# Optimization experiments

Hardware: AMD Instinct MI355X
Metric: run time of the kernel (lower is better)

The kernel has to match this reference:

```python
import jax, jax.numpy as jnp
import numpy as np

N_NODES = 102400   # 256 graphs x 400 nodes
N_EDGES = 1638400  # avg degree 16
C_IN = 128
C_OUT = 128
N_SAGE = 3         # gnn_num
G = 256            # num graphs
M = 400            # nodes per graph (equal-sized -> to_dense_batch is a reshape)


def setup_inputs() -> dict:
    key = jax.random.key(0)
    ks = jax.random.split(key, 6)
    x = jax.random.normal(ks[0], (N_NODES, C_IN), dtype=jnp.float32)
    edge_index = jax.random.randint(ks[1], (2, N_EDGES), 0, N_NODES, dtype=jnp.int32)
    # nodes sorted by graph id, equal graph sizes (matches to_dense_batch assumptions)
    batch = (jnp.arange(N_NODES, dtype=jnp.int32) // M)
    s_in = 1.0 / np.sqrt(C_IN)
    s_out = 1.0 / np.sqrt(C_OUT)
    W_g = jax.random.normal(ks[2], (C_IN, C_OUT), dtype=jnp.float32) * s_in
    b_g = jnp.zeros((C_OUT,), dtype=jnp.float32)
    W_l = jax.random.normal(ks[3], (N_SAGE, C_OUT, C_OUT), dtype=jnp.float32) * s_out  # neighbor lin
    b_l = jnp.zeros((N_SAGE, C_OUT), dtype=jnp.float32)
    W_r = jax.random.normal(ks[4], (N_SAGE, C_OUT, C_OUT), dtype=jnp.float32) * s_out  # root lin (no bias in PyG)
    return {"x": x, "W_g": W_g, "b_g": b_g, "W_l": W_l, "b_l": b_l,
            "W_r": W_r, "edge_index": edge_index, "batch": batch}


def _gcn_conv(x, W, b, src, dst):
    # PyG GCNConv: h = x W; add self loops; norm = d^{-1/2}_src * d^{-1/2}_dst,
    # deg = in-degree at dst counting the self loop; aggregate at dst; add bias.
    h = x @ W                                                     # [N, C_out]
    ones = jnp.ones((N_EDGES,), dtype=h.dtype)
    deg = jax.ops.segment_sum(ones, dst, num_segments=N_NODES) + 1.0
    dinv = jax.lax.rsqrt(deg)                                     # [N]
    norm = dinv[src] * dinv[dst]                                  # [E]
    agg = jax.ops.segment_sum(h[src] * norm[:, None], dst, num_segments=N_NODES)
    agg = agg + h * (dinv * dinv)[:, None]                        # self-loop term
    return agg + b


def _sage_conv(x, W_l, b_l, W_r, src, dst):
    # PyG SAGEConv (mean aggr): out = mean_{j in N(i)} x_j @ W_l + b_l + x @ W_r
    ones = jnp.ones((N_EDGES,), dtype=x.dtype)
    cnt = jax.ops.segment_sum(ones, dst, num_segments=N_NODES)
    s = jax.ops.segment_sum(x[src], dst, num_segments=N_NODES)
    mean = s / jnp.maximum(cnt, 1.0)[:, None]
    return mean @ W_l + b_l + x @ W_r


def _to_dense(x):
    # equal-sized graphs with nodes sorted by batch -> to_dense_batch == reshape
    return x.reshape(G, M, C_OUT)


def reference(x, W_g, b_g, W_l, b_l, W_r, edge_index, batch):
    src, dst = edge_index[0], edge_index[1]
    x = jax.nn.relu(_gcn_conv(x, W_g, b_g, src, dst))
    outs = [_to_dense(x)]
    for i in range(N_SAGE):
        x = jax.nn.relu(_sage_conv(x, W_l[i], b_l[i], W_r[i], src, dst))
        outs.append(_to_dense(x))
    return jnp.stack(outs)  # [N_SAGE+1, G, M, C_OUT]
```

## Files before the change

kernel.cpp:

```cpp
#include <hip/hip_runtime.h>

#define C 128
#define SLOT 64
typedef __attribute__((ext_vector_type(8))) short bf16x8;
typedef __attribute__((ext_vector_type(4))) float f32x4;

__device__ __forceinline__ unsigned short f2bf_rtn(float f) {
    unsigned u = __float_as_uint(f);
    return (unsigned short)((u + 0x7fff + ((u >> 16) & 1)) >> 16);
}
__device__ __forceinline__ float bflo(unsigned u) { return __uint_as_float(u << 16); }
__device__ __forceinline__ float bfhi(unsigned u) { return __uint_as_float(u & 0xffff0000u); }

__device__ __forceinline__ void gload_lds16(const unsigned short* g, unsigned short* l) {
    __builtin_amdgcn_global_load_lds(
        (const __attribute__((address_space(1))) void*)g,
        (__attribute__((address_space(3))) void*)l, 16, 0, 0);
}

__device__ __forceinline__ void split_bf16(float w, unsigned short& hb, unsigned short& lb) {
    unsigned u = __float_as_uint(w);
    hb = (unsigned short)(u >> 16);
    float hf = __uint_as_float(u & 0xffff0000u);
    lb = (unsigned short)(__float_as_uint(w - hf) >> 16);
}

__global__ __launch_bounds__(256) void wprep_all(const float* __restrict__ Wg,
        const float* __restrict__ Wl, const float* __restrict__ Wr,
        unsigned short* __restrict__ dstG, unsigned short* __restrict__ dstF,
        int* __restrict__ deg, int n) {
    int idx = blockIdx.x * 256 + threadIdx.x;
    if (idx < n) deg[idx] = 0;
    if (idx < 16384) {
        int k64 = idx & 63, ch = (idx >> 6) & 127, chunk = idx >> 13;
        int k = chunk * 64 + k64;
        unsigned short hb, lb;
        split_bf16(Wg[(size_t)k * 128 + ch], hb, lb);
        int pos = (((k64 >> 3) ^ (ch & 7)) << 3) | (k64 & 7);
        size_t base = ((size_t)chunk * 2) * 8192 + ch * 64 + pos;
        dstG[base] = hb;
        dstG[base + 8192] = lb;
    }
    int fidx = idx - 16384;
    if (fidx >= 0 && fidx < 3 * 4 * 128 * 64) {
        int k64 = fidx & 63, ch = (fidx >> 6) & 127, chunk = (fidx >> 13) & 3,
            layer = fidx >> 15;
        int k = chunk * 64 + k64;
        float w = (k < 128) ? Wl[((size_t)layer * 128 + k) * 128 + ch]
                            : Wr[((size_t)layer * 128 + (k - 128)) * 128 + ch];
        int pos = (((k64 >> 3) ^ (ch & 7)) << 3) | (k64 & 7);
        dstF[(((size_t)layer * 4 + chunk)) * 8192 + ch * 64 + pos] = f2bf_rtn(w);
    }
}

__global__ __launch_bounds__(256) void build_gemm_kernel(
        const int* __restrict__ ei, int* __restrict__ deg, int* __restrict__ rank, int E,
        const float* __restrict__ x, const unsigned short* __restrict__ Wp,
        unsigned short* __restrict__ outbf) {
    __shared__ unsigned short Bs[2][128][64];
    const int b2 = blockIdx.x >> 1;
    const int t = threadIdx.x;

    if (!(blockIdx.x & 1)) {
        const int base = b2 * 1024 + t * 4;
        int4 d4 = *(const int4*)(ei + E + base);
        int4 r;
        r.x = atomicAdd(&deg[d4.x], 1);
        r.y = atomicAdd(&deg[d4.y], 1);
        r.z = atomicAdd(&deg[d4.z], 1);
        r.w = atomicAdd(&deg[d4.w], 1);
        *(int4*)(rank + base) = r;
        return;
    }

    unsigned short* BsFlat = &Bs[0][0][0];
    const int lane = t & 63;
    const int wv = t >> 6;
    const int rowbase = b2 * 64 + wv * 16;
    const int arow = rowbase + (lane & 15);
    const int kq = lane >> 4;

    f32x4 acc[8];
#pragma unroll
    for (int f = 0; f < 8; f++) acc[f] = (f32x4){0.f, 0.f, 0.f, 0.f};

#pragma unroll
    for (int c = 0; c < 2; c++) {
        __syncthreads();
        {
            const unsigned short* srcW = Wp + (size_t)c * 16384;
#pragma unroll
            for (int i = 0; i < 8; i++)
                gload_lds16(srcW + (wv * 8 + i) * 512 + lane * 8,
                            BsFlat + (wv * 8 + i) * 512);
        }
        bf16x8 Ah[2], Al[2];
#pragma unroll
        for (int j = 0; j < 2; j++) {
            const float* base = x + (size_t)arow * C + c * 64 + j * 32;
            float4 x0 = ((const float4*)base)[kq * 2];
            float4 x1 = ((const float4*)base)[kq * 2 + 1];
            float xv[8] = {x0.x, x0.y, x0.z, x0.w, x1.x, x1.y, x1.z, x1.w};
#pragma unroll
            for (int q = 0; q < 8; q++) {
                unsigned u = __float_as_uint(xv[q]);
                Ah[j][q] = (short)(u >> 16);
                float hf = __uint_as_float(u & 0xffff0000u);
                Al[j][q] = (short)(__float_as_uint(xv[q] - hf) >> 16);
            }
        }
        __syncthreads();
#pragma unroll
        for (int j = 0; j < 2; j++) {
#pragma unroll
            for (int f = 0; f < 8; f++) {
                const int chh = f * 16 + (lane & 15);
                const int uu = (j * 4 + kq) ^ (lane & 7);
                bf16x8 bh = *(const bf16x8*)&Bs[0][chh][uu * 8];
                bf16x8 bl = *(const bf16x8*)&Bs[1][chh][uu * 8];
                acc[f] = __builtin_amdgcn_mfma_f32_16x16x32_bf16(Ah[j], bh, acc[f], 0, 0, 0);
                acc[f] = __builtin_amdgcn_mfma_f32_16x16x32_bf16(Al[j], bh, acc[f], 0, 0, 0);
                acc[f] = __builtin_amdgcn_mfma_f32_16x16x32_bf16(Ah[j], bl, acc[f], 0, 0, 0);
            }
        }
    }
    const int col = lane & 15;
    const int rq = lane >> 4;
#pragma unroll
    for (int f = 0; f < 8; f++)
#pragma unroll
        for (int j = 0; j < 4; j++) {
            const size_t o = (size_t)(rowbase + rq * 4 + j) * C + f * 16 + col;
            outbf[o] = f2bf_rtn(acc[f][j]);
        }
}

__global__ __launch_bounds__(256) void scatter_scale_kernel(
        const int* __restrict__ ei, const int* __restrict__ rank,
        int* __restrict__ csr, int E, const int* __restrict__ deg,
        unsigned short* __restrict__ tbl, float* __restrict__ dinv,
        float* __restrict__ cinv, int n) {
    const int SB = E >> 10;
    const int t = threadIdx.x;
    if (blockIdx.x < SB) {
        const int base = blockIdx.x * 1024 + t * 4;
        int4 s4 = *(const int4*)(ei + base);
        int4 d4 = *(const int4*)(ei + E + base);
        int4 r4 = *(const int4*)(rank + base);
        if (r4.x < SLOT) csr[(d4.x << 6) + r4.x] = s4.x;
        if (r4.y < SLOT) csr[(d4.y << 6) + r4.y] = s4.y;
        if (r4.z < SLOT) csr[(d4.z << 6) + r4.z] = s4.z;
        if (r4.w < SLOT) csr[(d4.w << 6) + r4.w] = s4.w;
        return;
    }
    const int rb = (blockIdx.x - SB) * 16 + (t >> 4);
    if (rb >= n) return;
    const int ch = (t & 15) * 8;
    const int d = deg[rb];
    const float di = rsqrtf((float)(d + 1));
    if ((t & 15) == 0) {
        dinv[rb] = di;
        cinv[rb] = 1.0f / (float)max(d, 1);
    }
    unsigned short* row = tbl + (size_t)rb * C + ch;
    uint4 v = *(const uint4*)row;
    uint4 w;
    w.x = (unsigned)f2bf_rtn(bflo(v.x) * di) | ((unsigned)f2bf_rtn(bfhi(v.x) * di) << 16);
    w.y = (unsigned)f2bf_rtn(bflo(v.y) * di) | ((unsigned)f2bf_rtn(bfhi(v.y) * di) << 16);
    w.z = (unsigned)f2bf_rtn(bflo(v.z) * di) | ((unsigned)f2bf_rtn(bfhi(v.z) * di) << 16);
    w.w = (unsigned)f2bf_rtn(bflo(v.w) * di) | ((unsigned)f2bf_rtn(bfhi(v.w) * di) << 16);
    *(uint4*)row = w;
}

template<int WBF>
__global__ __launch_bounds__(256) void gemm_sage(
        const unsigned short* __restrict__ Xbf, const unsigned short* __restrict__ Mbf,
        const unsigned short* __restrict__ Wp, const float* __restrict__ bias,
        float* __restrict__ outf, unsigned short* __restrict__ outbf) {
    __shared__ unsigned short Bs[128][64];
    unsigned short* BsFlat = &Bs[0][0];
    const int t = threadIdx.x;
    const int lane = t & 63;
    const int wv = t >> 6;
    const int rowbase = blockIdx.x * 64 + wv * 16;
    const int arow = rowbase + (lane & 15);
    const int kq = lane >> 4;

    f32x4 acc[8];
#pragma unroll
    for (int f = 0; f < 8; f++) acc[f] = (f32x4){0.f, 0.f, 0.f, 0.f};

#pragma unroll
    for (int c = 0; c < 4; c++) {
        __syncthreads();
        {
            const unsigned short* srcW = Wp + (size_t)c * 8192;
#pragma unroll
            for (int i = 0; i < 4; i++)
                gload_lds16(srcW + (wv * 4 + i) * 512 + lane * 8,
                            BsFlat + (wv * 4 + i) * 512);
        }
        const unsigned short* tab = (c < 2) ? Mbf : Xbf;
        bf16x8 Ah[2];
#pragma unroll
        for (int j = 0; j < 2; j++)
            Ah[j] = *(const bf16x8*)(tab + (size_t)arow * C + (c & 1) * 64 + j * 32 + kq * 8);
        __syncthreads();
#pragma unroll
        for (int j = 0; j < 2; j++) {
#pragma unroll
            for (int f = 0; f < 8; f++) {
                const int chh = f * 16 + (lane & 15);
                const int uu = (j * 4 + kq) ^ (lane & 7);
                bf16x8 bh = *(const bf16x8*)&Bs[chh][uu * 8];
                acc[f] = __builtin_amdgcn_mfma_f32_16x16x32_bf16(Ah[j], bh, acc[f], 0, 0, 0);
            }
        }
    }
    const int col = lane & 15;
    const int rq = lane >> 4;
#pragma unroll
    for (int f = 0; f < 8; f++) {
        const float b = bias[f * 16 + col];
#pragma unroll
        for (int j = 0; j < 4; j++) {
            const size_t o = (size_t)(rowbase + rq * 4 + j) * C + f * 16 + col;
            float v = fmaxf(acc[f][j] + b, 0.f);
            outf[o] = v;
            if (WBF) outbf[o] = f2bf_rtn(v);
        }
    }
}

template<int SELF, int BIASRELU, int WF, int WBF>
__global__ __launch_bounds__(256) void agg_kernel(
        const unsigned short* __restrict__ tbl, const int* __restrict__ csr,
        const int* __restrict__ deg, const float* __restrict__ scale,
        const float* __restrict__ bias, float* __restrict__ outf,
        unsigned short* __restrict__ outbf, int n) {
    const int lane = threadIdx.x & 63;
    const int qi = lane & 15;
    const int i = blockIdx.x * 16 + (threadIdx.x >> 6) * 4 + (lane >> 4);
    if (i >= n) return;
    const int dcount = min(deg[i], SLOT);
    const int b = i << 6;
    const int c8 = qi * 8;
    float a0 = 0.f, a1 = 0.f, a2 = 0.f, a3 = 0.f;
    float a4 = 0.f, a5 = 0.f, a6 = 0.f, a7 = 0.f;
#define ACC8(v) do { \
        a0 += bflo(v.x); a1 += bfhi(v.x); a2 += bflo(v.y); a3 += bfhi(v.y); \
        a4 += bflo(v.z); a5 += bfhi(v.z); a6 += bflo(v.w); a7 += bfhi(v.w); } while (0)
    for (int base = 0; base < dcount; base += 16) {
        const int cnt = min(16, dcount - base);
        int idx = (base + qi < dcount) ? csr[b + base + qi] : 0;
        int p = 0;
        for (; p + 8 <= cnt; p += 8) {
            int s0 = __shfl(idx, (lane & 48) + p);
            int s1 = __shfl(idx, (lane & 48) + p + 1);
            int s2 = __shfl(idx, (lane & 48) + p + 2);
            int s3 = __shfl(idx, (lane & 48) + p + 3);
            int s4 = __shfl(idx, (lane & 48) + p + 4);
            int s5 = __shfl(idx, (lane & 48) + p + 5);
            int s6 = __shfl(idx, (lane & 48) + p + 6);
            int s7 = __shfl(idx, (lane & 48) + p + 7);
            uint4 v0 = *(const uint4*)(tbl + (size_t)s0 * C + c8);
            uint4 v1 = *(const uint4*)(tbl + (size_t)s1 * C + c8);
            uint4 v2 = *(const uint4*)(tbl + (size_t)s2 * C + c8);
            uint4 v3 = *(const uint4*)(tbl + (size_t)s3 * C + c8);
            uint4 v4 = *(const uint4*)(tbl + (size_t)s4 * C + c8);
            uint4 v5 = *(const uint4*)(tbl + (size_t)s5 * C + c8);
            uint4 v6 = *(const uint4*)(tbl + (size_t)s6 * C + c8);
            uint4 v7 = *(const uint4*)(tbl + (size_t)s7 * C + c8);
            ACC8(v0); ACC8(v1); ACC8(v2); ACC8(v3);
            ACC8(v4); ACC8(v5); ACC8(v6); ACC8(v7);
        }
        for (; p + 4 <= cnt; p += 4) {
            int s0 = __shfl(idx, (lane & 48) + p);
            int s1 = __shfl(idx, (lane & 48) + p + 1);
            int s2 = __shfl(idx, (lane & 48) + p + 2);
            int s3 = __shfl(idx, (lane & 48) + p + 3);
            uint4 v0 = *(const uint4*)(tbl + (size_t)s0 * C + c8);
            uint4 v1 = *(const uint4*)(tbl + (size_t)s1 * C + c8);
            uint4 v2 = *(const uint4*)(tbl + (size_t)s2 * C + c8);
            uint4 v3 = *(const uint4*)(tbl + (size_t)s3 * C + c8);
            ACC8(v0); ACC8(v1); ACC8(v2); ACC8(v3);
        }
        for (; p < cnt; p++) {
            int s = __shfl(idx, (lane & 48) + p);
            uint4 v = *(const uint4*)(tbl + (size_t)s * C + c8);
            ACC8(v);
        }
    }
#undef ACC8
    if (SELF) {
        uint4 h = *(const uint4*)(tbl + (size_t)i * C + c8);
        a0 += bflo(h.x); a1 += bfhi(h.x); a2 += bflo(h.y); a3 += bfhi(h.y);
        a4 += bflo(h.z); a5 += bfhi(h.z); a6 += bflo(h.w); a7 += bfhi(h.w);
    }
    const float sc = scale[i];
    a0 *= sc; a1 *= sc; a2 *= sc; a3 *= sc;
    a4 *= sc; a5 *= sc; a6 *= sc; a7 *= sc;
    if (BIASRELU) {
        float4 b0 = *(const float4*)(bias + c8);
        float4 b1 = *(const float4*)(bias + c8 + 4);
        a0 = fmaxf(a0 + b0.x, 0.f); a1 = fmaxf(a1 + b0.y, 0.f);
        a2 = fmaxf(a2 + b0.z, 0.f); a3 = fmaxf(a3 + b0.w, 0.f);
        a4 = fmaxf(a4 + b1.x, 0.f); a5 = fmaxf(a5 + b1.y, 0.f);
        a6 = fmaxf(a6 + b1.z, 0.f); a7 = fmaxf(a7 + b1.w, 0.f);
    }
    if (WF) {
        float4 r0; r0.x = a0; r0.y = a1; r0.z = a2; r0.w = a3;
        float4 r1; r1.x = a4; r1.y = a5; r1.z = a6; r1.w = a7;
        *(float4*)(outf + (size_t)i * C + c8) = r0;
        *(float4*)(outf + (size_t)i * C + c8 + 4) = r1;
    }
    if (WBF) {
        uint4 pk;
        pk.x = (unsigned)f2bf_rtn(a0) | ((unsigned)f2bf_rtn(a1) << 16);
        pk.y = (unsigned)f2bf_rtn(a2) | ((unsigned)f2bf_rtn(a3) << 16);
        pk.z = (unsigned)f2bf_rtn(a4) | ((unsigned)f2bf_rtn(a5) << 16);
        pk.w = (unsigned)f2bf_rtn(a6) | ((unsigned)f2bf_rtn(a7) << 16);
        *(uint4*)(outbf + (size_t)i * C + c8) = pk;
    }
}


extern "C" void kernel_launch(void* const* d_in, const int* in_sizes, int n_in,
                              void* d_out, int out_size, void* d_ws, size_t ws_size,
                              hipStream_t stream) {
    const float* x   = (const float*)d_in[0];
    const float* W_g = (const float*)d_in[1];
    const float* b_g = (const float*)d_in[2];
    const float* W_l = (const float*)d_in[3];
    const float* b_l = (const float*)d_in[4];
    const float* W_r = (const float*)d_in[5];
    const int*   ei  = (const int*)d_in[6];

    const int N = in_sizes[0] / C;
    const int E = in_sizes[6] / 2;
    const size_t NC = (size_t)N * C;

    char* ws = (char*)d_ws;
    unsigned short* meanbf = (unsigned short*)ws;
    int* rank = (int*)meanbf;
    unsigned short* tblA   = meanbf + NC;
    unsigned short* tblB   = tblA + NC;
    int* deg  = (int*)(tblB + NC);
    float* dinv = (float*)(deg + N);
    float* cinv = dinv + N;
    unsigned short* wsWg = (unsigned short*)(cinv + N);
    unsigned short* wsWf = wsWg + 32768;

    float* out0 = (float*)d_out;
    int* csr = (int*)(out0 + 3 * NC);

    wprep_all<<<448, 256, 0, stream>>>(W_g, W_l, W_r, wsWg, wsWf, deg, N);

    build_gemm_kernel<<<2 * (N / 64), 256, 0, stream>>>(ei, deg, rank, E,
                                                        x, wsWg, tblA);
    scatter_scale_kernel<<<(E >> 10) + N / 16, 256, 0, stream>>>(
        ei, rank, csr, E, deg, tblA, dinv, cinv, N);

    agg_kernel<1, 1, 1, 1><<<(N + 15) / 16, 256, 0, stream>>>(tblA, csr, deg, dinv,
                                                              b_g, out0, tblB, N);

    const unsigned short* tin[3] = {tblB, tblA, tblB};
    unsigned short* tout[3] = {tblA, tblB, nullptr};
    for (int l = 0; l < 3; l++) {
        float* yout = out0 + (size_t)(l + 1) * NC;
        agg_kernel<0, 0, 0, 1><<<(N + 15) / 16, 256, 0, stream>>>(
            tin[l], csr, deg, cinv, nullptr, nullptr, meanbf, N);
        if (l < 2)
            gemm_sage<1><<<N / 64, 256, 0, stream>>>(tin[l], meanbf,
                wsWf + (size_t)l * 32768, b_l + (size_t)l * C, yout, tout[l]);
        else
            gemm_sage<0><<<N / 64, 256, 0, stream>>>(tin[l], meanbf,
                wsWf + (size_t)l * 32768, b_l + (size_t)l * C, yout, nullptr);
    }
}
```

Baseline: 421.6 us.

## Fuse SAGE mean aggregation into the GEMM kernel via LDS staging

Each SAGE layer now runs a single fused kernel. It gathers neighbor rows for 64 nodes, writes the bf16 mean into a swizzled LDS tile, and feeds that tile straight into the MFMA GEMM. This removes the separate aggregation launch and the global round-trip of the mean buffer. The CSR moves from the output buffer into the workspace, and the GCN aggregation kernel is specialized, dropping its 4-wide remainder loop. In exchange the fused kernel uses more LDS, and the gather and GEMM phases no longer overlap across kernels, which may lower occupancy.

```diff
diff --git a/kernel.cpp b/kernel.cpp
--- a/kernel.cpp
+++ b/kernel.cpp
@@ -172,68 +172,7 @@
     *(uint4*)row = w;
 }
 
-template<int WBF>
-__global__ __launch_bounds__(256) void gemm_sage(
-        const unsigned short* __restrict__ Xbf, const unsigned short* __restrict__ Mbf,
-        const unsigned short* __restrict__ Wp, const float* __restrict__ bias,
-        float* __restrict__ outf, unsigned short* __restrict__ outbf) {
-    __shared__ unsigned short Bs[128][64];
-    unsigned short* BsFlat = &Bs[0][0];
-    const int t = threadIdx.x;
-    const int lane = t & 63;
-    const int wv = t >> 6;
-    const int rowbase = blockIdx.x * 64 + wv * 16;
-    const int arow = rowbase + (lane & 15);
-    const int kq = lane >> 4;
-
-    f32x4 acc[8];
-#pragma unroll
-    for (int f = 0; f < 8; f++) acc[f] = (f32x4){0.f, 0.f, 0.f, 0.f};
-
-#pragma unroll
-    for (int c = 0; c < 4; c++) {
-        __syncthreads();
-        {
-            const unsigned short* srcW = Wp + (size_t)c * 8192;
-#pragma unroll
-            for (int i = 0; i < 4; i++)
-                gload_lds16(srcW + (wv * 4 + i) * 512 + lane * 8,
-                            BsFlat + (wv * 4 + i) * 512);
-        }
-        const unsigned short* tab = (c < 2) ? Mbf : Xbf;
-        bf16x8 Ah[2];
-#pragma unroll
-        for (int j = 0; j < 2; j++)
-            Ah[j] = *(const bf16x8*)(tab + (size_t)arow * C + (c & 1) * 64 + j * 32 + kq * 8);
-        __syncthreads();
-#pragma unroll
-        for (int j = 0; j < 2; j++) {
-#pragma unroll
-            for (int f = 0; f < 8; f++) {
-                const int chh = f * 16 + (lane & 15);
-                const int uu = (j * 4 + kq) ^ (lane & 7);
-                bf16x8 bh = *(const bf16x8*)&Bs[chh][uu * 8];
-                acc[f] = __builtin_amdgcn_mfma_f32_16x16x32_bf16(Ah[j], bh, acc[f], 0, 0, 0);
-            }
-        }
-    }
-    const int col = lane & 15;
-    const int rq = lane >> 4;
-#pragma unroll
-    for (int f = 0; f < 8; f++) {
-        const float b = bias[f * 16 + col];
-#pragma unroll
-        for (int j = 0; j < 4; j++) {
-            const size_t o = (size_t)(rowbase + rq * 4 + j) * C + f * 16 + col;
-            float v = fmaxf(acc[f][j] + b, 0.f);
-            outf[o] = v;
-            if (WBF) outbf[o] = f2bf_rtn(v);
-        }
-    }
-}
-
-template<int SELF, int BIASRELU, int WF, int WBF>
-__global__ __launch_bounds__(256) void agg_kernel(
+__global__ __launch_bounds__(256) void agg_gcn(
         const unsigned short* __restrict__ tbl, const int* __restrict__ csr,
         const int* __restrict__ deg, const float* __restrict__ scale,
         const float* __restrict__ bias, float* __restrict__ outf,
@@ -274,17 +213,6 @@
             ACC8(v0); ACC8(v1); ACC8(v2); ACC8(v3);
             ACC8(v4); ACC8(v5); ACC8(v6); ACC8(v7);
         }
-        for (; p + 4 <= cnt; p += 4) {
-            int s0 = __shfl(idx, (lane & 48) + p);
-            int s1 = __shfl(idx, (lane & 48) + p + 1);
-            int s2 = __shfl(idx, (lane & 48) + p + 2);
-            int s3 = __shfl(idx, (lane & 48) + p + 3);
-            uint4 v0 = *(const uint4*)(tbl + (size_t)s0 * C + c8);
-            uint4 v1 = *(const uint4*)(tbl + (size_t)s1 * C + c8);
-            uint4 v2 = *(const uint4*)(tbl + (size_t)s2 * C + c8);
-            uint4 v3 = *(const uint4*)(tbl + (size_t)s3 * C + c8);
-            ACC8(v0); ACC8(v1); ACC8(v2); ACC8(v3);
-        }
         for (; p < cnt; p++) {
             int s = __shfl(idx, (lane & 48) + p);
             uint4 v = *(const uint4*)(tbl + (size_t)s * C + c8);
@@ -292,35 +220,151 @@
         }
     }
 #undef ACC8
-    if (SELF) {
+    {
         uint4 h = *(const uint4*)(tbl + (size_t)i * C + c8);
         a0 += bflo(h.x); a1 += bfhi(h.x); a2 += bflo(h.y); a3 += bfhi(h.y);
         a4 += bflo(h.z); a5 += bfhi(h.z); a6 += bflo(h.w); a7 += bfhi(h.w);
     }
     const float sc = scale[i];
-    a0 *= sc; a1 *= sc; a2 *= sc; a3 *= sc;
-    a4 *= sc; a5 *= sc; a6 *= sc; a7 *= sc;
-    if (BIASRELU) {
-        float4 b0 = *(const float4*)(bias + c8);
-        float4 b1 = *(const float4*)(bias + c8 + 4);
-        a0 = fmaxf(a0 + b0.x, 0.f); a1 = fmaxf(a1 + b0.y, 0.f);
-        a2 = fmaxf(a2 + b0.z, 0.f); a3 = fmaxf(a3 + b0.w, 0.f);
-        a4 = fmaxf(a4 + b1.x, 0.f); a5 = fmaxf(a5 + b1.y, 0.f);
-        a6 = fmaxf(a6 + b1.z, 0.f); a7 = fmaxf(a7 + b1.w, 0.f);
-    }
-    if (WF) {
-        float4 r0; r0.x = a0; r0.y = a1; r0.z = a2; r0.w = a3;
-        float4 r1; r1.x = a4; r1.y = a5; r1.z = a6; r1.w = a7;
-        *(float4*)(outf + (size_t)i * C + c8) = r0;
-        *(float4*)(outf + (size_t)i * C + c8 + 4) = r1;
-    }
-    if (WBF) {
+    float4 b0 = *(const float4*)(bias + c8);
+    float4 b1 = *(const float4*)(bias + c8 + 4);
+    a0 = fmaxf(a0 * sc + b0.x, 0.f); a1 = fmaxf(a1 * sc + b0.y, 0.f);
+    a2 = fmaxf(a2 * sc + b0.z, 0.f); a3 = fmaxf(a3 * sc + b0.w, 0.f);
+    a4 = fmaxf(a4 * sc + b1.x, 0.f); a5 = fmaxf(a5 * sc + b1.y, 0.f);
+    a6 = fmaxf(a6 * sc + b1.z, 0.f); a7 = fmaxf(a7 * sc + b1.w, 0.f);
+    float4 r0; r0.x = a0; r0.y = a1; r0.z = a2; r0.w = a3;
+    float4 r1; r1.x = a4; r1.y = a5; r1.z = a6; r1.w = a7;
+    *(float4*)(outf + (size_t)i * C + c8) = r0;
+    *(float4*)(outf + (size_t)i * C + c8 + 4) = r1;
+    uint4 pk;
+    pk.x = (unsigned)f2bf_rtn(a0) | ((unsigned)f2bf_rtn(a1) << 16);
+    pk.y = (unsigned)f2bf_rtn(a2) | ((unsigned)f2bf_rtn(a3) << 16);
+    pk.z = (unsigned)f2bf_rtn(a4) | ((unsigned)f2bf_rtn(a5) << 16);
+    pk.w = (unsigned)f2bf_rtn(a6) | ((unsigned)f2bf_rtn(a7) << 16);
+    *(uint4*)(outbf + (size_t)i * C + c8) = pk;
+}
+
+template<int WBF>
+__global__ __launch_bounds__(256, 5) void fused_sage(
+        const unsigned short* __restrict__ tbl, const int* __restrict__ csr,
+        const int* __restrict__ deg, const float* __restrict__ cinv,
+        const unsigned short* __restrict__ Wp, const float* __restrict__ bias,
+        float* __restrict__ outf, unsigned short* __restrict__ outbf) {
+    __shared__ unsigned short Bs[128][64];
+    __shared__ unsigned short meanL[64][128];
+    unsigned short* BsFlat = &Bs[0][0];
+    const int t = threadIdx.x;
+    const int lane = t & 63;
+    const int wv = t >> 6;
+    const int qi = lane & 15;
+    const int qrow = lane >> 4;
+
+    for (int rr = 0; rr < 4; rr++) {
+        const int rloc = wv * 16 + rr * 4 + qrow;
+        const int gi = blockIdx.x * 64 + rloc;
+        const int dcount = min(deg[gi], SLOT);
+        const int b = gi << 6;
+        const int c8 = qi * 8;
+        float a0 = 0.f, a1 = 0.f, a2 = 0.f, a3 = 0.f;
+        float a4 = 0.f, a5 = 0.f, a6 = 0.f, a7 = 0.f;
+#define ACC8(v) do { \
+        a0 += bflo(v.x); a1 += bfhi(v.x); a2 += bflo(v.y); a3 += bfhi(v.y); \
+        a4 += bflo(v.z); a5 += bfhi(v.z); a6 += bflo(v.w); a7 += bfhi(v.w); } while (0)
+        for (int base = 0; base < dcount; base += 16) {
+            const int cnt = min(16, dcount - base);
+            int idx = (base + qi < dcount) ? csr[b + base + qi] : 0;
+            int p = 0;
+            for (; p + 8 <= cnt; p += 8) {
+                int s0 = __shfl(idx, (lane & 48) + p);
+                int s1 = __shfl(idx, (lane & 48) + p + 1);
+                int s2 = __shfl(idx, (lane & 48) + p + 2);
+                int s3 = __shfl(idx, (lane & 48) + p + 3);
+                int s4 = __shfl(idx, (lane & 48) + p + 4);
+                int s5 = __shfl(idx, (lane & 48) + p + 5);
+                int s6 = __shfl(idx, (lane & 48) + p + 6);
+                int s7 = __shfl(idx, (lane & 48) + p + 7);
+                uint4 v0 = *(const uint4*)(tbl + (size_t)s0 * C + c8);
+                uint4 v1 = *(const uint4*)(tbl + (size_t)s1 * C + c8);
+                uint4 v2 = *(const uint4*)(tbl + (size_t)s2 * C + c8);
+                uint4 v3 = *(const uint4*)(tbl + (size_t)s3 * C + c8);
+                uint4 v4 = *(const uint4*)(tbl + (size_t)s4 * C + c8);
+                uint4 v5 = *(const uint4*)(tbl + (size_t)s5 * C + c8);
+                uint4 v6 = *(const uint4*)(tbl + (size_t)s6 * C + c8);
+                uint4 v7 = *(const uint4*)(tbl + (size_t)s7 * C + c8);
+                ACC8(v0); ACC8(v1); ACC8(v2); ACC8(v3);
+                ACC8(v4); ACC8(v5); ACC8(v6); ACC8(v7);
+            }
+            for (; p < cnt; p++) {
+                int s = __shfl(idx, (lane & 48) + p);
+                uint4 v = *(const uint4*)(tbl + (size_t)s * C + c8);
+                ACC8(v);
+            }
+        }
+#undef ACC8
+        const float sc = cinv[gi];
+        a0 *= sc; a1 *= sc; a2 *= sc; a3 *= sc;
+        a4 *= sc; a5 *= sc; a6 *= sc; a7 *= sc;
         uint4 pk;
         pk.x = (unsigned)f2bf_rtn(a0) | ((unsigned)f2bf_rtn(a1) << 16);
         pk.y = (unsigned)f2bf_rtn(a2) | ((unsigned)f2bf_rtn(a3) << 16);
         pk.z = (unsigned)f2bf_rtn(a4) | ((unsigned)f2bf_rtn(a5) << 16);
         pk.w = (unsigned)f2bf_rtn(a6) | ((unsigned)f2bf_rtn(a7) << 16);
-        *(uint4*)(outbf + (size_t)i * C + c8) = pk;
+        *(uint4*)((char*)&meanL[rloc][0] + ((qi ^ (rloc & 7)) << 4)) = pk;
+    }
+
+    const int arow_loc = wv * 16 + (lane & 15);
+    const int arow = blockIdx.x * 64 + arow_loc;
+    const int kq = lane >> 4;
+    const int rowbase = blockIdx.x * 64 + wv * 16;
+
+    f32x4 acc[8];
+#pragma unroll
+    for (int f = 0; f < 8; f++) acc[f] = (f32x4){0.f, 0.f, 0.f, 0.f};
+
+#pragma unroll
+    for (int c = 0; c < 4; c++) {
+        __syncthreads();
+        {
+            const unsigned short* srcW = Wp + (size_t)c * 8192;
+#pragma unroll
+            for (int i = 0; i < 4; i++)
+                gload_lds16(srcW + (wv * 4 + i) * 512 + lane * 8,
+                            BsFlat + (wv * 4 + i) * 512);
+        }
+        bf16x8 Ah[2];
+#pragma unroll
+        for (int j = 0; j < 2; j++) {
+            if (c < 2) {
+                const int u = (c * 8 + j * 4 + kq) ^ (arow_loc & 7);
+                Ah[j] = *(const bf16x8*)((const char*)&meanL[arow_loc][0] + u * 16);
+            } else {
+                Ah[j] = *(const bf16x8*)(tbl + (size_t)arow * C + (c & 1) * 64 + j * 32 + kq * 8);
+            }
+        }
+        __syncthreads();
+#pragma unroll
+        for (int j = 0; j < 2; j++) {
+#pragma unroll
+            for (int f = 0; f < 8; f++) {
+                const int chh = f * 16 + (lane & 15);
+                const int uu = (j * 4 + kq) ^ (lane & 7);
+                bf16x8 bh = *(const bf16x8*)&Bs[chh][uu * 8];
+                acc[f] = __builtin_amdgcn_mfma_f32_16x16x32_bf16(Ah[j], bh, acc[f], 0, 0, 0);
+            }
+        }
+    }
+    const int col = lane & 15;
+    const int rq = lane >> 4;
+#pragma unroll
+    for (int f = 0; f < 8; f++) {
+        const float b = bias[f * 16 + col];
+#pragma unroll
+        for (int j = 0; j < 4; j++) {
+            const size_t o = (size_t)(rowbase + rq * 4 + j) * C + f * 16 + col;
+            float v = fmaxf(acc[f][j] + b, 0.f);
+            outf[o] = v;
+            if (WBF) outbf[o] = f2bf_rtn(v);
+        }
     }
 }
 
@@ -341,18 +385,17 @@
     const size_t NC = (size_t)N * C;
 
     char* ws = (char*)d_ws;
-    unsigned short* meanbf = (unsigned short*)ws;
-    int* rank = (int*)meanbf;
-    unsigned short* tblA   = meanbf + NC;
-    unsigned short* tblB   = tblA + NC;
-    int* deg  = (int*)(tblB + NC);
+    unsigned short* tblA = (unsigned short*)ws;
+    unsigned short* tblB = tblA + NC;
+    int* rank = (int*)tblB;
+    int* csr  = (int*)(tblB + NC);
+    int* deg  = csr + (size_t)N * SLOT;
     float* dinv = (float*)(deg + N);
     float* cinv = dinv + N;
     unsigned short* wsWg = (unsigned short*)(cinv + N);
     unsigned short* wsWf = wsWg + 32768;
 
     float* out0 = (float*)d_out;
-    int* csr = (int*)(out0 + 3 * NC);
 
     wprep_all<<<448, 256, 0, stream>>>(W_g, W_l, W_r, wsWg, wsWf, deg, N);
 
@@ -361,20 +404,18 @@
     scatter_scale_kernel<<<(E >> 10) + N / 16, 256, 0, stream>>>(
         ei, rank, csr, E, deg, tblA, dinv, cinv, N);
 
-    agg_kernel<1, 1, 1, 1><<<(N + 15) / 16, 256, 0, stream>>>(tblA, csr, deg, dinv,
-                                                              b_g, out0, tblB, N);
+    agg_gcn<<<(N + 15) / 16, 256, 0, stream>>>(tblA, csr, deg, dinv,
+                                               b_g, out0, tblB, N);
 
     const unsigned short* tin[3] = {tblB, tblA, tblB};
     unsigned short* tout[3] = {tblA, tblB, nullptr};
     for (int l = 0; l < 3; l++) {
         float* yout = out0 + (size_t)(l + 1) * NC;
-        agg_kernel<0, 0, 0, 1><<<(N + 15) / 16, 256, 0, stream>>>(
-            tin[l], csr, deg, cinv, nullptr, nullptr, meanbf, N);
         if (l < 2)
-            gemm_sage<1><<<N / 64, 256, 0, stream>>>(tin[l], meanbf,
+            fused_sage<1><<<N / 64, 256, 0, stream>>>(tin[l], csr, deg, cinv,
                 wsWf + (size_t)l * 32768, b_l + (size_t)l * C, yout, tout[l]);
         else
-            gemm_sage<0><<<N / 64, 256, 0, stream>>>(tin[l], meanbf,
+            fused_sage<0><<<N / 64, 256, 0, stream>>>(tin[l], csr, deg, cinv,
                 wsWf + (size_t)l * 32768, b_l + (size_t)l * C, yout, nullptr);
     }
 }
```

After: 434.3 us. 1.03x slower.
